# Kernel optimization log

Measured on AMD Instinct MI355X. Metric: run time of the kernel, lower is better.

## Reference

```python
import jax, jax.numpy as jnp
import numpy as np

P, B, D, H, O = 512, 8, 256, 75, 128  # passage_len, batch, input_size, attn hidden, GRU hidden


def setup_inputs() -> dict:
    key = jax.random.key(0)
    ks = jax.random.split(key, 10)

    def w(k, shape, fan_in):
        return jax.random.normal(k, shape, jnp.float32) * (1.0 / np.sqrt(fan_in))

    return {
        "v": jax.random.normal(ks[0], (P, B, D), jnp.float32),
        "Wvp1": w(ks[1], (H, D), D),          # nn.Linear(input_size, hidden, bias=False)
        "Wvp2": w(ks[2], (H, D), D),
        "vw": w(ks[3], (H,), H),               # nn.Linear(hidden, 1, bias=False)
        "Wg": w(ks[4], (2 * D, 2 * D), 2 * D),  # Gate linear, no bias
        "w_ih_f": w(ks[5], (3 * O, 2 * D), 2 * D),
        "w_hh_f": w(ks[6], (3 * O, O), O),
        "b_ih_f": jnp.zeros((3 * O,), jnp.float32),
        "b_hh_f": jnp.zeros((3 * O,), jnp.float32),
        "w_ih_b": w(ks[7], (3 * O, 2 * D), 2 * D),
        "w_hh_b": w(ks[8], (3 * O, O), O),
        "b_ih_b": jnp.zeros((3 * O,), jnp.float32),
        "b_hh_b": jnp.zeros((3 * O,), jnp.float32),
    }


def _gru(x, w_ih, w_hh, b_ih, b_hh):
    # x: (T, B, in) -> hidden states (T, B, O); PyTorch GRU gate order (r, z, n)
    hdim = w_hh.shape[1]
    xp = x @ w_ih.T + b_ih  # precompute input projections: (T, B, 3O)

    def step(h, xp_t):
        gh = h @ w_hh.T + b_hh
        i_r, i_z, i_n = jnp.split(xp_t, 3, axis=-1)
        h_r, h_z, h_n = jnp.split(gh, 3, axis=-1)
        r = jax.nn.sigmoid(i_r + h_r)
        z = jax.nn.sigmoid(i_z + h_z)
        n = jnp.tanh(i_n + r * h_n)
        h_new = (1.0 - z) * n + z * h
        return h_new, h_new

    h0 = jnp.zeros((x.shape[1], hdim), x.dtype)
    _, hs = jax.lax.scan(step, h0, xp)
    return hs


def reference(v, Wvp1, Wvp2, vw, Wg,
              w_ih_f, w_hh_f, b_ih_f, b_hh_f,
              w_ih_b, w_hh_b, b_ih_b, b_hh_b):
    # dropout is inference no-op (and in the torch code its result is discarded anyway)
    Wv1 = v @ Wvp1.T  # (P, B, H) -- broadcast over key axis (dim 1 after expand)
    Wv2 = v @ Wvp2.T  # (P, B, H) -- broadcast over query axis
    # s[i, j, b, h] = tanh(Wv2[i] + Wv1[j]); softmax over i (keys)
    s = jnp.tanh(Wv2[:, None] + Wv1[None, :])          # (P, P, B, H)
    scores = jnp.einsum('ijbh,h->ijb', s, vw)          # (P, P, B)
    a = jax.nn.softmax(scores, axis=0)
    c = jnp.einsum('ijb,ibd->jbd', a, v)               # attended context (P, B, D)
    g = jnp.concatenate([v, c], axis=2)                # (P, B, 2D)
    g = jax.nn.sigmoid(g @ Wg.T) * g                   # Gate
    hf = _gru(g, w_ih_f, w_hh_f, b_ih_f, b_hh_f)
    hb = _gru(g[::-1], w_ih_b, w_hh_b, b_ih_b, b_hh_b)[::-1]
    return jnp.concatenate([hf, hb], axis=2)           # (P, B, 2O)
```

## Files before the change

kernel.cpp:

```cpp
#include <hip/hip_runtime.h>

#define TP 512
#define TB 8
#define TD 256
#define TH 75
#define THP 80
#define TO 128

#define LOG2E2 2.8853900817779268f

typedef _Float16 half_t;
typedef _Float16 half2v __attribute__((ext_vector_type(2)));
typedef _Float16 half4v __attribute__((ext_vector_type(4)));
typedef _Float16 half8v __attribute__((ext_vector_type(8)));
typedef float    float4v __attribute__((ext_vector_type(4)));

__device__ __forceinline__ float fast_rcp(float x) { return __builtin_amdgcn_rcpf(x); }
__device__ __forceinline__ float ex2(float x) {
#if __has_builtin(__builtin_amdgcn_exp2f)
    return __builtin_amdgcn_exp2f(x);
#else
    float r; asm("v_exp_f32 %0, %1" : "=v"(r) : "v"(x)); return r;
#endif
}
__device__ __forceinline__ float fast_tanh(float x) {
    return 1.0f - 2.0f * fast_rcp(1.0f + __expf(2.0f * x));
}
__device__ __forceinline__ float fast_sigmoid(float x) {
    return fast_rcp(1.0f + __expf(-x));
}
__device__ __forceinline__ float fdot2h(half2v a, half2v b, float c) {
#if __has_builtin(__builtin_amdgcn_fdot2)
    return __builtin_amdgcn_fdot2(a, b, c, false);
#else
    return c + (float)a[0] * (float)b[0] + (float)a[1] * (float)b[1];
#endif
}
#define EXT2(v, j) __builtin_shufflevector((v), (v), 2*(j), 2*(j)+1)
__device__ __forceinline__ void dot3_h8(half8v wr, half8v wz, half8v wn, half8v h,
                                        float& ar, float& az, float& an) {
    half2v h0 = EXT2(h, 0), h1 = EXT2(h, 1), h2 = EXT2(h, 2), h3 = EXT2(h, 3);
    ar = fdot2h(EXT2(wr, 0), h0, ar);
    az = fdot2h(EXT2(wz, 0), h0, az);
    an = fdot2h(EXT2(wn, 0), h0, an);
    ar = fdot2h(EXT2(wr, 1), h1, ar);
    az = fdot2h(EXT2(wz, 1), h1, az);
    an = fdot2h(EXT2(wn, 1), h1, an);
    ar = fdot2h(EXT2(wr, 2), h2, ar);
    az = fdot2h(EXT2(wz, 2), h2, az);
    an = fdot2h(EXT2(wn, 2), h2, an);
    ar = fdot2h(EXT2(wr, 3), h3, ar);
    az = fdot2h(EXT2(wz, 3), h3, az);
    an = fdot2h(EXT2(wn, 3), h3, an);
}
__device__ __forceinline__ float pair_sum_dpp(float v) {
    int i1 = __builtin_amdgcn_update_dpp(0, __builtin_bit_cast(int, v), 0xB1, 0xF, 0xF, true);
    return v + __builtin_bit_cast(float, i1);
}

__global__ __launch_bounds__(256) void prep_kernel(
    const float* __restrict__ v,
    const float* __restrict__ Wvp1, const float* __restrict__ Wvp2,
    const float* __restrict__ Wg,   const float* __restrict__ wihf,
    const float* __restrict__ wihb, const float* __restrict__ bihf,
    const float* __restrict__ bihb, const float* __restrict__ whhf,
    const float* __restrict__ whhb,
    float* __restrict__ bihC,
    half_t* __restrict__ v16, half_t* __restrict__ g16,
    half_t* __restrict__ Wg16B, half_t* __restrict__ Wih16B,
    half_t* __restrict__ whh16, half_t* __restrict__ WT16B,
    half_t* __restrict__ vT16)
{
    __shared__ half_t lt[64 * 66];

    if (blockIdx.x >= 7203) {
        int vb = blockIdx.x - 7203;
        int t = threadIdx.x;
        int b  = vb >> 5;
        int pt = (vb >> 2) & 7;
        int dt = vb & 3;
        {
            int pl = t >> 2, dseg = (t & 3) * 16;
            const float4* src = (const float4*)(v + (((pt * 64 + pl) * 8 + b) << 8) + dt * 64 + dseg);
            float4 f0 = src[0], f1 = src[1], f2 = src[2], f3 = src[3];
            half_t hv[16] = {
                (half_t)f0.x,(half_t)f0.y,(half_t)f0.z,(half_t)f0.w,
                (half_t)f1.x,(half_t)f1.y,(half_t)f1.z,(half_t)f1.w,
                (half_t)f2.x,(half_t)f2.y,(half_t)f2.z,(half_t)f2.w,
                (half_t)f3.x,(half_t)f3.y,(half_t)f3.z,(half_t)f3.w };
#pragma unroll
            for (int u = 0; u < 16; ++u) lt[(dseg + u) * 66 + pl] = hv[u];
        }
        __syncthreads();
        {
            int dl = t >> 2, pseg = (t & 3) * 16;
            half8v h0 = *(const half8v*)(lt + dl * 66 + pseg);
            half8v h1 = *(const half8v*)(lt + dl * 66 + pseg + 8);
            half8v* dst = (half8v*)(vT16 + ((b * 256 + dt * 64 + dl) << 9) + pt * 64 + pseg);
            dst[0] = h0; dst[1] = h1;
        }
        return;
    }

    int idx = blockIdx.x * 256 + threadIdx.x;
    if (idx < 1048576) {
        half_t val = (half_t)v[idx];
        v16[idx] = val;
        int row = idx >> 8, d = idx & 255;
        g16[row * 512 + d] = val;
        return;
    }
    idx -= 1048576;
    if (idx < 768) { bihC[idx] = (idx < 384) ? bihf[idx] : bihb[idx - 384]; return; }
    idx -= 768;
    if (idx < 262144) {
        int j = idx & 7, lane = (idx >> 3) & 63, kt = (idx >> 9) & 15, nt = idx >> 13;
        int o = nt * 16 + (lane & 15);
        int k = kt * 32 + ((lane >> 4) << 3) + j;
        Wg16B[idx] = (half_t)Wg[o * 512 + k];
        return;
    }
    idx -= 262144;
    if (idx < 393216) {
        int j = idx & 7, lane = (idx >> 3) & 63, kt = (idx >> 9) & 15, nt = idx >> 13;
        int o = nt * 16 + (lane & 15);
        int k = kt * 32 + ((lane >> 4) << 3) + j;
        Wih16B[idx] = (half_t)((o < 384) ? wihf[o * 512 + k] : wihb[(o - 384) * 512 + k]);
        return;
    }
    idx -= 393216;
    if (idx < 98304) {
        int d = idx / 49152, i = idx - d * 49152;
        whh16[idx] = (half_t)(d ? whhb[i] : whhf[i]);
        return;
    }
    idx -= 98304;
    if (idx < 40960) {
        int j = idx & 7, lane = (idx >> 3) & 63, kt = (idx >> 9) & 7, nt = idx >> 12;
        int o = nt * 16 + (lane & 15);
        int k = kt * 32 + ((lane >> 4) << 3) + j;
        float vv = 0.0f;
        if (o < 75)       vv = Wvp1[o * 256 + k];
        else if (o < 150) vv = Wvp2[(o - 75) * 256 + k];
        WT16B[idx] = (half_t)vv;
    }
}

__global__ __launch_bounds__(128) void wv12_kernel(
    const half_t* __restrict__ v16, const half_t* __restrict__ WT16B,
    float* __restrict__ Wv1, float* __restrict__ Wv2T)
{
    int tid = threadIdx.x;
    int lane = tid & 63, w = tid >> 6;
    int l15 = lane & 15, quad = lane >> 4;
    int r0 = blockIdx.x * 16;

    float4v acc[5];
#pragma unroll
    for (int n5 = 0; n5 < 5; ++n5) acc[n5] = (float4v){0.f, 0.f, 0.f, 0.f};

#pragma unroll
    for (int kt = 0; kt < 8; ++kt) {
        half8v a = *(const half8v*)(v16 + (r0 + l15) * 256 + kt * 32 + quad * 8);
#pragma unroll
        for (int n5 = 0; n5 < 5; ++n5) {
            int nt = w * 5 + n5;
            half8v b = *(const half8v*)(WT16B + ((nt * 8 + kt) * 64 + lane) * 8);
            acc[n5] = __builtin_amdgcn_mfma_f32_16x16x32_f16(a, b, acc[n5], 0, 0, 0);
        }
    }
#pragma unroll
    for (int n5 = 0; n5 < 5; ++n5) {
        int col = (w * 5 + n5) * 16 + l15;
#pragma unroll
        for (int r = 0; r < 4; ++r) {
            int row = r0 + quad * 4 + r;
            int p = row >> 3, b = row & 7;
            int ob = (b * TP + p) * THP;
            float val2 = LOG2E2 * acc[n5][r];
            if (col < 75)       Wv1[ob + col] = val2;
            else if (col < 80)  { Wv1[ob + col] = 0.0f;
                                  Wv2T[(b * THP + col - 75) * TP + p] = val2; }
            else if (col < 150) Wv2T[(b * THP + col - 75) * TP + p] = val2;
            else if (col < 155) Wv2T[(b * THP + col - 75) * TP + p] = 0.0f;
        }
    }
}

__global__ __launch_bounds__(256) void score_kernel(
    const float* __restrict__ Wv1, const float* __restrict__ Wv2T,
    const float* __restrict__ vw, half_t* __restrict__ a16)
{
    int tid = threadIdx.x;
    int b  = blockIdx.x >> 7;
    int j0 = (blockIdx.x & 127) * 4;
    __shared__ float wv1j[4 * THP];
    __shared__ float vws[THP];
    __shared__ float sc[4 * TP];

    if (tid < THP) vws[tid] = (tid < TH) ? vw[tid] : 0.0f;
    for (int e = tid; e < 4 * THP; e += 256) {
        int jj = e / THP, k = e - jj * THP;
        wv1j[e] = Wv1[(b * TP + j0 + jj) * THP + k];
    }
    __syncthreads();

    float Csum = 0.0f;
    {
        const float4* c4 = (const float4*)vws;
        for (int kk = 0; kk < 20; ++kk) { float4 c = c4[kk]; Csum += c.x + c.y + c.z + c.w; }
    }

    int i0 = tid, i1 = tid + 256;
    float acc0[4] = {0.f,0.f,0.f,0.f}, acc1[4] = {0.f,0.f,0.f,0.f};
    const float* wvt = Wv2T + b * THP * TP;
#pragma unroll
    for (int kt = 0; kt < 5; ++kt) {
        float r0v[16], r1v[16];
#pragma unroll
        for (int u = 0; u < 16; ++u) {
            const float* colp = wvt + (kt * 16 + u) * TP;
            r0v[u] = colp[i0];
            r1v[u] = colp[i1];
        }
        const float* cp = vws + kt * 16;
#pragma unroll
        for (int jj = 0; jj < 4; ++jj) {
            const float* w1 = wv1j + jj * THP + kt * 16;
            float s0 = 0.f, s1 = 0.f;
#pragma unroll
            for (int u = 0; u < 16; ++u) {
                float cu = cp[u], wu = w1[u];
                s0 += cu * fast_rcp(1.0f + ex2(r0v[u] + wu));
                s1 += cu * fast_rcp(1.0f + ex2(r1v[u] + wu));
            }
            acc0[jj] += s0; acc1[jj] += s1;
        }
    }
#pragma unroll
    for (int jj = 0; jj < 4; ++jj) {
        sc[jj * TP + i0] = Csum - 2.0f * acc0[jj];
        sc[jj * TP + i1] = Csum - 2.0f * acc1[jj];
    }
    __syncthreads();

    {
        int jj = tid >> 6, l = tid & 63;
        float m = -1e30f;
#pragma unroll
        for (int q = 0; q < 8; ++q) m = fmaxf(m, sc[jj * TP + l + q * 64]);
#pragma unroll
        for (int s = 32; s > 0; s >>= 1) m = fmaxf(m, __shfl_xor(m, s));
        float e[8];
        float sum = 0.0f;
#pragma unroll
        for (int q = 0; q < 8; ++q) { e[q] = __expf(sc[jj * TP + l + q * 64] - m); sum += e[q]; }
#pragma unroll
        for (int s = 32; s > 0; s >>= 1) sum += __shfl_xor(sum, s);
        float inv = fast_rcp(sum);
        half_t* arow = a16 + (b * TP + j0 + jj) * TP;
#pragma unroll
        for (int q = 0; q < 8; ++q) arow[l + q * 64] = (half_t)(e[q] * inv);
    }
}

__global__ __launch_bounds__(256) void context_kernel(
    const half_t* __restrict__ a16, const half_t* __restrict__ vT16,
    half_t* __restrict__ g16)
{
    int tid = threadIdx.x;
    int lane = tid & 63, w = tid >> 6;
    int l15 = lane & 15, quad = lane >> 4;
    int b  = blockIdx.x >> 5;
    int mt = blockIdx.x & 31;

    const half_t* arow = a16 + (b * TP + mt * 16 + l15) * TP;
    const half_t* vbase = vT16 + ((b * 256) << 9);

    float4v acc[4];
#pragma unroll
    for (int nti = 0; nti < 4; ++nti) acc[nti] = (float4v){0.f, 0.f, 0.f, 0.f};

#pragma unroll 4
    for (int kt = 0; kt < 16; ++kt) {
        half8v a = *(const half8v*)(arow + kt * 32 + quad * 8);
#pragma unroll
        for (int nti = 0; nti < 4; ++nti) {
            int d = (w * 4 + nti) * 16 + l15;
            half8v bb = *(const half8v*)(vbase + (d << 9) + kt * 32 + quad * 8);
            acc[nti] = __builtin_amdgcn_mfma_f32_16x16x32_f16(a, bb, acc[nti], 0, 0, 0);
        }
    }
#pragma unroll
    for (int nti = 0; nti < 4; ++nti) {
        int d = (w * 4 + nti) * 16 + l15;
#pragma unroll
        for (int r = 0; r < 4; ++r) {
            int j = mt * 16 + quad * 4 + r;
            g16[(j * TB + b) * 512 + 256 + d] = (half_t)acc[nti][r];
        }
    }
}

__global__ __launch_bounds__(256, 1) void gatexp_kernel(
    const half_t* __restrict__ g16, const half_t* __restrict__ Wg16B,
    const half_t* __restrict__ Wih16B, const float* __restrict__ bihC,
    float* __restrict__ xpf, float* __restrict__ xpb)
{
    __shared__ half_t gA[32 * 520];
    int tid = threadIdx.x;
    int r0 = blockIdx.x * 32;
    int lane = tid & 63, w = tid >> 6;
    int l15 = lane & 15, quad = lane >> 4;

    for (int e = tid; e < 2048; e += 256) {
        int row = e >> 6, c8 = e & 63;
        *(half8v*)(gA + row * 520 + c8 * 8) =
            *(const half8v*)(g16 + (r0 + row) * 512 + c8 * 8);
    }
    __syncthreads();

    float4v acc[2][8];
#pragma unroll
    for (int mi = 0; mi < 2; ++mi)
#pragma unroll
        for (int nti = 0; nti < 8; ++nti) acc[mi][nti] = (float4v){0.f, 0.f, 0.f, 0.f};

    for (int kt = 0; kt < 16; ++kt) {
        half8v a0 = *(const half8v*)(gA + l15 * 520 + kt * 32 + quad * 8);
        half8v a1 = *(const half8v*)(gA + (16 + l15) * 520 + kt * 32 + quad * 8);
#pragma unroll
        for (int nti = 0; nti < 8; ++nti) {
            half8v bb = *(const half8v*)(Wg16B + (((w * 8 + nti) * 16 + kt) * 64 + lane) * 8);
            acc[0][nti] = __builtin_amdgcn_mfma_f32_16x16x32_f16(a0, bb, acc[0][nti], 0, 0, 0);
            acc[1][nti] = __builtin_amdgcn_mfma_f32_16x16x32_f16(a1, bb, acc[1][nti], 0, 0, 0);
        }
    }
#pragma unroll
    for (int mi = 0; mi < 2; ++mi)
#pragma unroll
        for (int nti = 0; nti < 8; ++nti) {
            int colg = (w * 8 + nti) * 16 + l15;
#pragma unroll
            for (int r = 0; r < 4; ++r) {
                float gv = (float)gA[(mi * 16 + quad * 4 + r) * 520 + colg];
                acc[mi][nti][r] = fast_sigmoid(acc[mi][nti][r]) * gv;
            }
        }
    __syncthreads();
#pragma unroll
    for (int mi = 0; mi < 2; ++mi)
#pragma unroll
        for (int nti = 0; nti < 8; ++nti) {
            int colg = (w * 8 + nti) * 16 + l15;
#pragma unroll
            for (int r = 0; r < 4; ++r)
                gA[(mi * 16 + quad * 4 + r) * 520 + colg] = (half_t)acc[mi][nti][r];
        }
    __syncthreads();

    float4v c2[2][12];
#pragma unroll
    for (int mi = 0; mi < 2; ++mi)
#pragma unroll
        for (int nt2 = 0; nt2 < 12; ++nt2) {
            float bv = bihC[(w * 12 + nt2) * 16 + l15];
            c2[mi][nt2] = (float4v){bv, bv, bv, bv};
        }

    for (int kt = 0; kt < 16; ++kt) {
        half8v a0 = *(const half8v*)(gA + l15 * 520 + kt * 32 + quad * 8);
        half8v a1 = *(const half8v*)(gA + (16 + l15) * 520 + kt * 32 + quad * 8);
#pragma unroll
        for (int nt2 = 0; nt2 < 12; ++nt2) {
            half8v bb = *(const half8v*)(Wih16B + (((w * 12 + nt2) * 16 + kt) * 64 + lane) * 8);
            c2[0][nt2] = __builtin_amdgcn_mfma_f32_16x16x32_f16(a0, bb, c2[0][nt2], 0, 0, 0);
            c2[1][nt2] = __builtin_amdgcn_mfma_f32_16x16x32_f16(a1, bb, c2[1][nt2], 0, 0, 0);
        }
    }
#pragma unroll
    for (int mi = 0; mi < 2; ++mi)
#pragma unroll
        for (int nt2 = 0; nt2 < 12; ++nt2) {
            int col = (w * 12 + nt2) * 16 + l15;
            float* dst = (col < 384) ? (xpf + col) : (xpb + col - 384);
#pragma unroll
            for (int r = 0; r < 4; ++r)
                dst[(r0 + mi * 16 + quad * 4 + r) * 384] = c2[mi][nt2][r];
        }
}

__global__ __launch_bounds__(256, 1) void gru_kernel(
    const float* __restrict__ xpf, const float* __restrict__ xpb,
    const half_t* __restrict__ whh16,
    const float* __restrict__ bhhf, const float* __restrict__ bhhb,
    float* __restrict__ out)
{
    int tid = threadIdx.x;
    int dir = blockIdx.x >> 3;
    int b   = blockIdx.x & 7;
    const float* xp  = dir ? xpb  : xpf;
    const float* bhh = dir ? bhhb : bhhf;
    const half_t* wbase = whh16 + dir * 3 * TO * TO;

    __shared__ __align__(16) half_t hb[2][TO];

    int o = tid >> 1, hf = tid & 1;

    half8v wr[8], wz[8], wn[8];
    {
        const half_t* pr = wbase + (o)          * TO + hf * 64;
        const half_t* pz = wbase + (TO + o)     * TO + hf * 64;
        const half_t* pn = wbase + (2 * TO + o) * TO + hf * 64;
        asm volatile(
            "global_load_dwordx4 %0,  %24, off\n\t"
            "global_load_dwordx4 %1,  %24, off offset:16\n\t"
            "global_load_dwordx4 %2,  %24, off offset:32\n\t"
            "global_load_dwordx4 %3,  %24, off offset:48\n\t"
            "global_load_dwordx4 %4,  %24, off offset:64\n\t"
            "global_load_dwordx4 %5,  %24, off offset:80\n\t"
            "global_load_dwordx4 %6,  %24, off offset:96\n\t"
            "global_load_dwordx4 %7,  %24, off offset:112\n\t"
            "global_load_dwordx4 %8,  %25, off\n\t"
            "global_load_dwordx4 %9,  %25, off offset:16\n\t"
            "global_load_dwordx4 %10, %25, off offset:32\n\t"
            "global_load_dwordx4 %11, %25, off offset:48\n\t"
            "global_load_dwordx4 %12, %25, off offset:64\n\t"
            "global_load_dwordx4 %13, %25, off offset:80\n\t"
            "global_load_dwordx4 %14, %25, off offset:96\n\t"
            "global_load_dwordx4 %15, %25, off offset:112\n\t"
            "global_load_dwordx4 %16, %26, off\n\t"
            "global_load_dwordx4 %17, %26, off offset:16\n\t"
            "global_load_dwordx4 %18, %26, off offset:32\n\t"
            "global_load_dwordx4 %19, %26, off offset:48\n\t"
            "global_load_dwordx4 %20, %26, off offset:64\n\t"
            "global_load_dwordx4 %21, %26, off offset:80\n\t"
            "global_load_dwordx4 %22, %26, off offset:96\n\t"
            "global_load_dwordx4 %23, %26, off offset:112\n\t"
            "s_waitcnt vmcnt(0)"
            : "=&v"(wr[0]), "=&v"(wr[1]), "=&v"(wr[2]), "=&v"(wr[3]),
              "=&v"(wr[4]), "=&v"(wr[5]), "=&v"(wr[6]), "=&v"(wr[7]),
              "=&v"(wz[0]), "=&v"(wz[1]), "=&v"(wz[2]), "=&v"(wz[3]),
              "=&v"(wz[4]), "=&v"(wz[5]), "=&v"(wz[6]), "=&v"(wz[7]),
              "=&v"(wn[0]), "=&v"(wn[1]), "=&v"(wn[2]), "=&v"(wn[3]),
              "=&v"(wn[4]), "=&v"(wn[5]), "=&v"(wn[6]), "=&v"(wn[7])
            : "v"(pr), "v"(pz), "v"(pn));
    }

    float br = 0.f, bz = 0.f, bn = 0.f, h = 0.f;
    if (hf == 0) {
        br = bhh[o]; bz = bhh[TO + o]; bn = bhh[2 * TO + o];
    }
    if (tid < TO) hb[0][tid] = (half_t)0.0f;
    __syncthreads();

    float xrv[8], xzv[8], xnv[8], hist[8];

    for (int S = 0; S < TP; S += 8) {
        if (hf == 0) {
#pragma unroll
            for (int u = 0; u < 8; ++u) {
                int s = S + u;
                int tn = dir ? (TP - 1 - s) : s;
                const float* xpt = xp + (tn * TB + b) * 384;
                xrv[u] = xpt[o]; xzv[u] = xpt[TO + o]; xnv[u] = xpt[2 * TO + o];
            }
        }
#pragma unroll
        for (int u = 0; u < 8; ++u) {
            int s = S + u;
            int cur = s & 1;
            const half8v* h8 = (const half8v*)(&hb[cur][hf * 64]);
            half8v hv0 = h8[0], hv1 = h8[1], hv2 = h8[2], hv3 = h8[3];
            half8v hv4 = h8[4], hv5 = h8[5], hv6 = h8[6], hv7 = h8[7];

            float ar = 0.f, az = 0.f, an = 0.f;
            dot3_h8(wr[0], wz[0], wn[0], hv0, ar, az, an);
            dot3_h8(wr[1], wz[1], wn[1], hv1, ar, az, an);
            dot3_h8(wr[2], wz[2], wn[2], hv2, ar, az, an);
            dot3_h8(wr[3], wz[3], wn[3], hv3, ar, az, an);
            dot3_h8(wr[4], wz[4], wn[4], hv4, ar, az, an);
            dot3_h8(wr[5], wz[5], wn[5], hv5, ar, az, an);
            dot3_h8(wr[6], wz[6], wn[6], hv6, ar, az, an);
            dot3_h8(wr[7], wz[7], wn[7], hv7, ar, az, an);

            ar = pair_sum_dpp(ar);
            az = pair_sum_dpp(az);
            an = pair_sum_dpp(an);
            if (hf == 0) {
                float r = fast_sigmoid(xrv[u] + ar + br);
                float z = fast_sigmoid(xzv[u] + az + bz);
                float n = fast_tanh(xnv[u] + r * (an + bn));
                h = (1.0f - z) * n + z * h;
                hb[cur ^ 1][o] = (half_t)h;
                hist[u] = h;
            }
            asm volatile("s_waitcnt lgkmcnt(0)" ::: "memory");
            __builtin_amdgcn_s_barrier();
        }
        if (hf == 0) {
#pragma unroll
            for (int u = 0; u < 8; ++u) {
                int s = S + u;
                int t = dir ? (TP - 1 - s) : s;
                out[(t * TB + b) * 256 + dir * TO + o] = hist[u];
            }
        }
    }
}

extern "C" void kernel_launch(void* const* d_in, const int* in_sizes, int n_in,
                              void* d_out, int out_size, void* d_ws, size_t ws_size,
                              hipStream_t stream) {
    const float* v    = (const float*)d_in[0];
    const float* Wvp1 = (const float*)d_in[1];
    const float* Wvp2 = (const float*)d_in[2];
    const float* vw   = (const float*)d_in[3];
    const float* Wg   = (const float*)d_in[4];
    const float* wihf = (const float*)d_in[5];
    const float* whhf = (const float*)d_in[6];
    const float* bihf = (const float*)d_in[7];
    const float* bhhf = (const float*)d_in[8];
    const float* wihb = (const float*)d_in[9];
    const float* whhb = (const float*)d_in[10];
    const float* bihb = (const float*)d_in[11];
    const float* bhhb = (const float*)d_in[12];

    float* ws   = (float*)d_ws;
    float* bihC = ws;
    float* Wv1  = bihC + 768;
    float* Wv2T = Wv1 + 327680;
    float* xpf  = Wv2T + 327680;
    float* xpb  = xpf + 1572864;
    half_t* g16    = (half_t*)(xpb + 1572864);
    half_t* Wg16B  = g16 + 2097152;
    half_t* Wih16B = Wg16B + 262144;
    half_t* whh16  = Wih16B + 393216;
    half_t* v16    = whh16 + 98304;
    half_t* WT16B  = v16 + 1048576;
    half_t* vT16   = WT16B + 40960;
    half_t* a16    = vT16 + 1048576;
    float* out  = (float*)d_out;

    prep_kernel<<<7459, 256, 0, stream>>>(v, Wvp1, Wvp2, Wg, wihf, wihb, bihf, bihb,
                                          whhf, whhb, bihC, v16, g16,
                                          Wg16B, Wih16B, whh16, WT16B, vT16);
    wv12_kernel<<<256, 128, 0, stream>>>(v16, WT16B, Wv1, Wv2T);
    score_kernel<<<1024, 256, 0, stream>>>(Wv1, Wv2T, vw, a16);
    context_kernel<<<256, 256, 0, stream>>>(a16, vT16, g16);
    gatexp_kernel<<<128, 256, 0, stream>>>(g16, Wg16B, Wih16B, bihC, xpf, xpb);
    gru_kernel<<<16, 256, 0, stream>>>(xpf, xpb, whh16, bhhf, bhhb, out);
}
```

Measured before the change: 417.0 us.

## Fuse attention and gate stages into one persistent kernel with grid barriers

Merges the wv12, score, context and gate/input-projection kernels into a single persistent 512-block kernel that separates the stages with software grid barriers built on atomics. Barrier counters are reset in the prep kernel. The intent is to remove three kernel launch gaps and their tail idle time. In exchange, the kernel depends on all 512 blocks being co-resident, since otherwise the barrier spin deadlocks. Later stages also leave many blocks idle (only 256 or 128 active), and launch_bounds(256,2) may constrain registers.

```diff
diff --git a/kernel.cpp b/kernel.cpp
--- a/kernel.cpp
+++ b/kernel.cpp
@@ -58,6 +58,20 @@
     return v + __builtin_bit_cast(float, i1);
 }
 
+__device__ __forceinline__ void grid_barrier(unsigned* cnt, unsigned* rel, unsigned nblk) {
+    __syncthreads();
+    if (threadIdx.x == 0) {
+        unsigned old = __hip_atomic_fetch_add(cnt, 1u, __ATOMIC_ACQ_REL, __HIP_MEMORY_SCOPE_AGENT);
+        if (old == nblk - 1u) {
+            __hip_atomic_store(rel, 1u, __ATOMIC_RELEASE, __HIP_MEMORY_SCOPE_AGENT);
+        } else {
+            while (__hip_atomic_load(rel, __ATOMIC_ACQUIRE, __HIP_MEMORY_SCOPE_AGENT) == 0u)
+                __builtin_amdgcn_s_sleep(2);
+        }
+    }
+    __syncthreads();
+}
+
 __global__ __launch_bounds__(256) void prep_kernel(
     const float* __restrict__ v,
     const float* __restrict__ Wvp1, const float* __restrict__ Wvp2,
@@ -69,9 +83,11 @@
     half_t* __restrict__ v16, half_t* __restrict__ g16,
     half_t* __restrict__ Wg16B, half_t* __restrict__ Wih16B,
     half_t* __restrict__ whh16, half_t* __restrict__ WT16B,
-    half_t* __restrict__ vT16)
+    half_t* __restrict__ vT16, unsigned* __restrict__ bar)
 {
     __shared__ half_t lt[64 * 66];
+
+    if (blockIdx.x == 0 && threadIdx.x < 8) bar[threadIdx.x] = 0u;
 
     if (blockIdx.x >= 7203) {
         int vb = blockIdx.x - 7203;
@@ -146,248 +162,240 @@
     }
 }
 
-__global__ __launch_bounds__(128) void wv12_kernel(
+__global__ __launch_bounds__(256, 2) void mid_kernel(
     const half_t* __restrict__ v16, const half_t* __restrict__ WT16B,
-    float* __restrict__ Wv1, float* __restrict__ Wv2T)
+    float* __restrict__ Wv1, float* __restrict__ Wv2T,
+    const float* __restrict__ vw, half_t* __restrict__ a16,
+    const half_t* __restrict__ vT16, half_t* __restrict__ g16,
+    const half_t* __restrict__ Wg16B, const half_t* __restrict__ Wih16B,
+    const float* __restrict__ bihC,
+    float* __restrict__ xpf, float* __restrict__ xpb,
+    unsigned* __restrict__ bar)
 {
+    __shared__ __align__(16) unsigned char smem[33280];
     int tid = threadIdx.x;
     int lane = tid & 63, w = tid >> 6;
     int l15 = lane & 15, quad = lane >> 4;
-    int r0 = blockIdx.x * 16;
-
-    float4v acc[5];
-#pragma unroll
-    for (int n5 = 0; n5 < 5; ++n5) acc[n5] = (float4v){0.f, 0.f, 0.f, 0.f};
-
-#pragma unroll
-    for (int kt = 0; kt < 8; ++kt) {
-        half8v a = *(const half8v*)(v16 + (r0 + l15) * 256 + kt * 32 + quad * 8);
-#pragma unroll
-        for (int n5 = 0; n5 < 5; ++n5) {
-            int nt = w * 5 + n5;
-            half8v b = *(const half8v*)(WT16B + ((nt * 8 + kt) * 64 + lane) * 8);
-            acc[n5] = __builtin_amdgcn_mfma_f32_16x16x32_f16(a, b, acc[n5], 0, 0, 0);
-        }
-    }
-#pragma unroll
-    for (int n5 = 0; n5 < 5; ++n5) {
-        int col = (w * 5 + n5) * 16 + l15;
-#pragma unroll
-        for (int r = 0; r < 4; ++r) {
-            int row = r0 + quad * 4 + r;
-            int p = row >> 3, b = row & 7;
-            int ob = (b * TP + p) * THP;
-            float val2 = LOG2E2 * acc[n5][r];
-            if (col < 75)       Wv1[ob + col] = val2;
-            else if (col < 80)  { Wv1[ob + col] = 0.0f;
-                                  Wv2T[(b * THP + col - 75) * TP + p] = val2; }
-            else if (col < 150) Wv2T[(b * THP + col - 75) * TP + p] = val2;
-            else if (col < 155) Wv2T[(b * THP + col - 75) * TP + p] = 0.0f;
-        }
-    }
-}
-
-__global__ __launch_bounds__(256) void score_kernel(
-    const float* __restrict__ Wv1, const float* __restrict__ Wv2T,
-    const float* __restrict__ vw, half_t* __restrict__ a16)
-{
-    int tid = threadIdx.x;
-    int b  = blockIdx.x >> 7;
-    int j0 = (blockIdx.x & 127) * 4;
-    __shared__ float wv1j[4 * THP];
-    __shared__ float vws[THP];
-    __shared__ float sc[4 * TP];
-
-    if (tid < THP) vws[tid] = (tid < TH) ? vw[tid] : 0.0f;
-    for (int e = tid; e < 4 * THP; e += 256) {
-        int jj = e / THP, k = e - jj * THP;
-        wv1j[e] = Wv1[(b * TP + j0 + jj) * THP + k];
-    }
-    __syncthreads();
-
-    float Csum = 0.0f;
+
     {
-        const float4* c4 = (const float4*)vws;
-        for (int kk = 0; kk < 20; ++kk) { float4 c = c4[kk]; Csum += c.x + c.y + c.z + c.w; }
-    }
-
-    int i0 = tid, i1 = tid + 256;
-    float acc0[4] = {0.f,0.f,0.f,0.f}, acc1[4] = {0.f,0.f,0.f,0.f};
-    const float* wvt = Wv2T + b * THP * TP;
-#pragma unroll
-    for (int kt = 0; kt < 5; ++kt) {
-        float r0v[16], r1v[16];
-#pragma unroll
-        for (int u = 0; u < 16; ++u) {
-            const float* colp = wvt + (kt * 16 + u) * TP;
-            r0v[u] = colp[i0];
-            r1v[u] = colp[i1];
-        }
-        const float* cp = vws + kt * 16;
-#pragma unroll
-        for (int jj = 0; jj < 4; ++jj) {
-            const float* w1 = wv1j + jj * THP + kt * 16;
-            float s0 = 0.f, s1 = 0.f;
-#pragma unroll
-            for (int u = 0; u < 16; ++u) {
-                float cu = cp[u], wu = w1[u];
-                s0 += cu * fast_rcp(1.0f + ex2(r0v[u] + wu));
-                s1 += cu * fast_rcp(1.0f + ex2(r1v[u] + wu));
-            }
-            acc0[jj] += s0; acc1[jj] += s1;
-        }
-    }
-#pragma unroll
-    for (int jj = 0; jj < 4; ++jj) {
-        sc[jj * TP + i0] = Csum - 2.0f * acc0[jj];
-        sc[jj * TP + i1] = Csum - 2.0f * acc1[jj];
-    }
-    __syncthreads();
+        int g = blockIdx.x * 4 + w;
+        for (int t = g; t < 2560; t += 2048) {
+            int rt = t / 10, nt = t - rt * 10;
+            int r0 = rt * 16;
+            float4v acc = (float4v){0.f, 0.f, 0.f, 0.f};
+#pragma unroll
+            for (int kt = 0; kt < 8; ++kt) {
+                half8v a = *(const half8v*)(v16 + (r0 + l15) * 256 + kt * 32 + quad * 8);
+                half8v b = *(const half8v*)(WT16B + ((nt * 8 + kt) * 64 + lane) * 8);
+                acc = __builtin_amdgcn_mfma_f32_16x16x32_f16(a, b, acc, 0, 0, 0);
+            }
+            int col = nt * 16 + l15;
+#pragma unroll
+            for (int r = 0; r < 4; ++r) {
+                int row = r0 + quad * 4 + r;
+                int p = row >> 3, b = row & 7;
+                int ob = (b * TP + p) * THP;
+                float val2 = LOG2E2 * acc[r];
+                if (col < 75)       Wv1[ob + col] = val2;
+                else if (col < 80)  { Wv1[ob + col] = 0.0f;
+                                      Wv2T[(b * THP + col - 75) * TP + p] = val2; }
+                else if (col < 150) Wv2T[(b * THP + col - 75) * TP + p] = val2;
+                else if (col < 155) Wv2T[(b * THP + col - 75) * TP + p] = 0.0f;
+            }
+        }
+    }
+    grid_barrier(bar + 0, bar + 1, 512);
 
     {
-        int jj = tid >> 6, l = tid & 63;
-        float m = -1e30f;
-#pragma unroll
-        for (int q = 0; q < 8; ++q) m = fmaxf(m, sc[jj * TP + l + q * 64]);
-#pragma unroll
-        for (int s = 32; s > 0; s >>= 1) m = fmaxf(m, __shfl_xor(m, s));
-        float e[8];
-        float sum = 0.0f;
-#pragma unroll
-        for (int q = 0; q < 8; ++q) { e[q] = __expf(sc[jj * TP + l + q * 64] - m); sum += e[q]; }
-#pragma unroll
-        for (int s = 32; s > 0; s >>= 1) sum += __shfl_xor(sum, s);
-        float inv = fast_rcp(sum);
-        half_t* arow = a16 + (b * TP + j0 + jj) * TP;
-#pragma unroll
-        for (int q = 0; q < 8; ++q) arow[l + q * 64] = (half_t)(e[q] * inv);
-    }
-}
-
-__global__ __launch_bounds__(256) void context_kernel(
-    const half_t* __restrict__ a16, const half_t* __restrict__ vT16,
-    half_t* __restrict__ g16)
-{
-    int tid = threadIdx.x;
-    int lane = tid & 63, w = tid >> 6;
-    int l15 = lane & 15, quad = lane >> 4;
-    int b  = blockIdx.x >> 5;
-    int mt = blockIdx.x & 31;
-
-    const half_t* arow = a16 + (b * TP + mt * 16 + l15) * TP;
-    const half_t* vbase = vT16 + ((b * 256) << 9);
-
-    float4v acc[4];
-#pragma unroll
-    for (int nti = 0; nti < 4; ++nti) acc[nti] = (float4v){0.f, 0.f, 0.f, 0.f};
+        float* wv1j = (float*)smem;
+        float* vws  = wv1j + 4 * THP;
+        float* sc   = vws + THP;
+        for (int t = blockIdx.x; t < 1024; t += 512) {
+            int b  = t >> 7;
+            int j0 = (t & 127) * 4;
+
+            if (tid < THP) vws[tid] = (tid < TH) ? vw[tid] : 0.0f;
+            for (int e = tid; e < 4 * THP; e += 256) {
+                int jj = e / THP, k = e - jj * THP;
+                wv1j[e] = Wv1[(b * TP + j0 + jj) * THP + k];
+            }
+            __syncthreads();
+
+            float Csum = 0.0f;
+            {
+                const float4* c4 = (const float4*)vws;
+                for (int kk = 0; kk < 20; ++kk) { float4 c = c4[kk]; Csum += c.x + c.y + c.z + c.w; }
+            }
+
+            int i0 = tid, i1 = tid + 256;
+            float acc0[4] = {0.f,0.f,0.f,0.f}, acc1[4] = {0.f,0.f,0.f,0.f};
+            const float* wvt = Wv2T + b * THP * TP;
+#pragma unroll
+            for (int kt = 0; kt < 5; ++kt) {
+                float r0v[16], r1v[16];
+#pragma unroll
+                for (int u = 0; u < 16; ++u) {
+                    const float* colp = wvt + (kt * 16 + u) * TP;
+                    r0v[u] = colp[i0];
+                    r1v[u] = colp[i1];
+                }
+                const float* cp = vws + kt * 16;
+#pragma unroll
+                for (int jj = 0; jj < 4; ++jj) {
+                    const float* w1 = wv1j + jj * THP + kt * 16;
+                    float s0 = 0.f, s1 = 0.f;
+#pragma unroll
+                    for (int u = 0; u < 16; ++u) {
+                        float cu = cp[u], wu = w1[u];
+                        s0 += cu * fast_rcp(1.0f + ex2(r0v[u] + wu));
+                        s1 += cu * fast_rcp(1.0f + ex2(r1v[u] + wu));
+                    }
+                    acc0[jj] += s0; acc1[jj] += s1;
+                }
+            }
+#pragma unroll
+            for (int jj = 0; jj < 4; ++jj) {
+                sc[jj * TP + i0] = Csum - 2.0f * acc0[jj];
+                sc[jj * TP + i1] = Csum - 2.0f * acc1[jj];
+            }
+            __syncthreads();
+
+            {
+                int jj = tid >> 6, l = tid & 63;
+                float m = -1e30f;
+#pragma unroll
+                for (int q = 0; q < 8; ++q) m = fmaxf(m, sc[jj * TP + l + q * 64]);
+#pragma unroll
+                for (int s = 32; s > 0; s >>= 1) m = fmaxf(m, __shfl_xor(m, s));
+                float e[8];
+                float sum = 0.0f;
+#pragma unroll
+                for (int q = 0; q < 8; ++q) { e[q] = __expf(sc[jj * TP + l + q * 64] - m); sum += e[q]; }
+#pragma unroll
+                for (int s = 32; s > 0; s >>= 1) sum += __shfl_xor(sum, s);
+                float inv = fast_rcp(sum);
+                half_t* arow = a16 + (b * TP + j0 + jj) * TP;
+#pragma unroll
+                for (int q = 0; q < 8; ++q) arow[l + q * 64] = (half_t)(e[q] * inv);
+            }
+            __syncthreads();
+        }
+    }
+    grid_barrier(bar + 2, bar + 3, 512);
+
+    if (blockIdx.x < 256) {
+        int b  = blockIdx.x >> 5;
+        int mt = blockIdx.x & 31;
+
+        const half_t* arow = a16 + (b * TP + mt * 16 + l15) * TP;
+        const half_t* vbase = vT16 + ((b * 256) << 9);
+
+        float4v acc[4];
+#pragma unroll
+        for (int nti = 0; nti < 4; ++nti) acc[nti] = (float4v){0.f, 0.f, 0.f, 0.f};
 
 #pragma unroll 4
-    for (int kt = 0; kt < 16; ++kt) {
-        half8v a = *(const half8v*)(arow + kt * 32 + quad * 8);
+        for (int kt = 0; kt < 16; ++kt) {
+            half8v a = *(const half8v*)(arow + kt * 32 + quad * 8);
+#pragma unroll
+            for (int nti = 0; nti < 4; ++nti) {
+                int d = (w * 4 + nti) * 16 + l15;
+                half8v bb = *(const half8v*)(vbase + (d << 9) + kt * 32 + quad * 8);
+                acc[nti] = __builtin_amdgcn_mfma_f32_16x16x32_f16(a, bb, acc[nti], 0, 0, 0);
+            }
+        }
 #pragma unroll
         for (int nti = 0; nti < 4; ++nti) {
             int d = (w * 4 + nti) * 16 + l15;
-            half8v bb = *(const half8v*)(vbase + (d << 9) + kt * 32 + quad * 8);
-            acc[nti] = __builtin_amdgcn_mfma_f32_16x16x32_f16(a, bb, acc[nti], 0, 0, 0);
-        }
-    }
-#pragma unroll
-    for (int nti = 0; nti < 4; ++nti) {
-        int d = (w * 4 + nti) * 16 + l15;
-#pragma unroll
-        for (int r = 0; r < 4; ++r) {
-            int j = mt * 16 + quad * 4 + r;
-            g16[(j * TB + b) * 512 + 256 + d] = (half_t)acc[nti][r];
-        }
-    }
-}
-
-__global__ __launch_bounds__(256, 1) void gatexp_kernel(
-    const half_t* __restrict__ g16, const half_t* __restrict__ Wg16B,
-    const half_t* __restrict__ Wih16B, const float* __restrict__ bihC,
-    float* __restrict__ xpf, float* __restrict__ xpb)
-{
-    __shared__ half_t gA[32 * 520];
-    int tid = threadIdx.x;
-    int r0 = blockIdx.x * 32;
-    int lane = tid & 63, w = tid >> 6;
-    int l15 = lane & 15, quad = lane >> 4;
-
-    for (int e = tid; e < 2048; e += 256) {
-        int row = e >> 6, c8 = e & 63;
-        *(half8v*)(gA + row * 520 + c8 * 8) =
-            *(const half8v*)(g16 + (r0 + row) * 512 + c8 * 8);
-    }
-    __syncthreads();
-
-    float4v acc[2][8];
-#pragma unroll
-    for (int mi = 0; mi < 2; ++mi)
-#pragma unroll
-        for (int nti = 0; nti < 8; ++nti) acc[mi][nti] = (float4v){0.f, 0.f, 0.f, 0.f};
-
-    for (int kt = 0; kt < 16; ++kt) {
-        half8v a0 = *(const half8v*)(gA + l15 * 520 + kt * 32 + quad * 8);
-        half8v a1 = *(const half8v*)(gA + (16 + l15) * 520 + kt * 32 + quad * 8);
-#pragma unroll
-        for (int nti = 0; nti < 8; ++nti) {
-            half8v bb = *(const half8v*)(Wg16B + (((w * 8 + nti) * 16 + kt) * 64 + lane) * 8);
-            acc[0][nti] = __builtin_amdgcn_mfma_f32_16x16x32_f16(a0, bb, acc[0][nti], 0, 0, 0);
-            acc[1][nti] = __builtin_amdgcn_mfma_f32_16x16x32_f16(a1, bb, acc[1][nti], 0, 0, 0);
-        }
-    }
-#pragma unroll
-    for (int mi = 0; mi < 2; ++mi)
-#pragma unroll
-        for (int nti = 0; nti < 8; ++nti) {
-            int colg = (w * 8 + nti) * 16 + l15;
 #pragma unroll
             for (int r = 0; r < 4; ++r) {
-                float gv = (float)gA[(mi * 16 + quad * 4 + r) * 520 + colg];
-                acc[mi][nti][r] = fast_sigmoid(acc[mi][nti][r]) * gv;
-            }
-        }
-    __syncthreads();
-#pragma unroll
-    for (int mi = 0; mi < 2; ++mi)
-#pragma unroll
-        for (int nti = 0; nti < 8; ++nti) {
-            int colg = (w * 8 + nti) * 16 + l15;
-#pragma unroll
-            for (int r = 0; r < 4; ++r)
-                gA[(mi * 16 + quad * 4 + r) * 520 + colg] = (half_t)acc[mi][nti][r];
-        }
-    __syncthreads();
-
-    float4v c2[2][12];
-#pragma unroll
-    for (int mi = 0; mi < 2; ++mi)
-#pragma unroll
-        for (int nt2 = 0; nt2 < 12; ++nt2) {
-            float bv = bihC[(w * 12 + nt2) * 16 + l15];
-            c2[mi][nt2] = (float4v){bv, bv, bv, bv};
-        }
-
-    for (int kt = 0; kt < 16; ++kt) {
-        half8v a0 = *(const half8v*)(gA + l15 * 520 + kt * 32 + quad * 8);
-        half8v a1 = *(const half8v*)(gA + (16 + l15) * 520 + kt * 32 + quad * 8);
-#pragma unroll
-        for (int nt2 = 0; nt2 < 12; ++nt2) {
-            half8v bb = *(const half8v*)(Wih16B + (((w * 12 + nt2) * 16 + kt) * 64 + lane) * 8);
-            c2[0][nt2] = __builtin_amdgcn_mfma_f32_16x16x32_f16(a0, bb, c2[0][nt2], 0, 0, 0);
-            c2[1][nt2] = __builtin_amdgcn_mfma_f32_16x16x32_f16(a1, bb, c2[1][nt2], 0, 0, 0);
-        }
-    }
-#pragma unroll
-    for (int mi = 0; mi < 2; ++mi)
-#pragma unroll
-        for (int nt2 = 0; nt2 < 12; ++nt2) {
-            int col = (w * 12 + nt2) * 16 + l15;
-            float* dst = (col < 384) ? (xpf + col) : (xpb + col - 384);
-#pragma unroll
-            for (int r = 0; r < 4; ++r)
-                dst[(r0 + mi * 16 + quad * 4 + r) * 384] = c2[mi][nt2][r];
-        }
+                int j = mt * 16 + quad * 4 + r;
+                g16[(j * TB + b) * 512 + 256 + d] = (half_t)acc[nti][r];
+            }
+        }
+    }
+    grid_barrier(bar + 4, bar + 5, 512);
+
+    if (blockIdx.x < 128) {
+        half_t* gA = (half_t*)smem;
+        int r0 = blockIdx.x * 32;
+
+        for (int e = tid; e < 2048; e += 256) {
+            int row = e >> 6, c8 = e & 63;
+            *(half8v*)(gA + row * 520 + c8 * 8) =
+                *(const half8v*)(g16 + (r0 + row) * 512 + c8 * 8);
+        }
+        __syncthreads();
+
+        float4v acc[2][8];
+#pragma unroll
+        for (int mi = 0; mi < 2; ++mi)
+#pragma unroll
+            for (int nti = 0; nti < 8; ++nti) acc[mi][nti] = (float4v){0.f, 0.f, 0.f, 0.f};
+
+        for (int kt = 0; kt < 16; ++kt) {
+            half8v a0 = *(const half8v*)(gA + l15 * 520 + kt * 32 + quad * 8);
+            half8v a1 = *(const half8v*)(gA + (16 + l15) * 520 + kt * 32 + quad * 8);
+#pragma unroll
+            for (int nti = 0; nti < 8; ++nti) {
+                half8v bb = *(const half8v*)(Wg16B + (((w * 8 + nti) * 16 + kt) * 64 + lane) * 8);
+                acc[0][nti] = __builtin_amdgcn_mfma_f32_16x16x32_f16(a0, bb, acc[0][nti], 0, 0, 0);
+                acc[1][nti] = __builtin_amdgcn_mfma_f32_16x16x32_f16(a1, bb, acc[1][nti], 0, 0, 0);
+            }
+        }
+#pragma unroll
+        for (int mi = 0; mi < 2; ++mi)
+#pragma unroll
+            for (int nti = 0; nti < 8; ++nti) {
+                int colg = (w * 8 + nti) * 16 + l15;
+#pragma unroll
+                for (int r = 0; r < 4; ++r) {
+                    float gv = (float)gA[(mi * 16 + quad * 4 + r) * 520 + colg];
+                    acc[mi][nti][r] = fast_sigmoid(acc[mi][nti][r]) * gv;
+                }
+            }
+        __syncthreads();
+#pragma unroll
+        for (int mi = 0; mi < 2; ++mi)
+#pragma unroll
+            for (int nti = 0; nti < 8; ++nti) {
+                int colg = (w * 8 + nti) * 16 + l15;
+#pragma unroll
+                for (int r = 0; r < 4; ++r)
+                    gA[(mi * 16 + quad * 4 + r) * 520 + colg] = (half_t)acc[mi][nti][r];
+            }
+        __syncthreads();
+
+        float4v c2[2][12];
+#pragma unroll
+        for (int mi = 0; mi < 2; ++mi)
+#pragma unroll
+            for (int nt2 = 0; nt2 < 12; ++nt2) {
+                float bv = bihC[(w * 12 + nt2) * 16 + l15];
+                c2[mi][nt2] = (float4v){bv, bv, bv, bv};
+            }
+
+        for (int kt = 0; kt < 16; ++kt) {
+            half8v a0 = *(const half8v*)(gA + l15 * 520 + kt * 32 + quad * 8);
+            half8v a1 = *(const half8v*)(gA + (16 + l15) * 520 + kt * 32 + quad * 8);
+#pragma unroll
+            for (int nt2 = 0; nt2 < 12; ++nt2) {
+                half8v bb = *(const half8v*)(Wih16B + (((w * 12 + nt2) * 16 + kt) * 64 + lane) * 8);
+                c2[0][nt2] = __builtin_amdgcn_mfma_f32_16x16x32_f16(a0, bb, c2[0][nt2], 0, 0, 0);
+                c2[1][nt2] = __builtin_amdgcn_mfma_f32_16x16x32_f16(a1, bb, c2[1][nt2], 0, 0, 0);
+            }
+        }
+#pragma unroll
+        for (int mi = 0; mi < 2; ++mi)
+#pragma unroll
+            for (int nt2 = 0; nt2 < 12; ++nt2) {
+                int col = (w * 12 + nt2) * 16 + l15;
+                float* dst = (col < 384) ? (xpf + col) : (xpb + col - 384);
+#pragma unroll
+                for (int r = 0; r < 4; ++r)
+                    dst[(r0 + mi * 16 + quad * 4 + r) * 384] = c2[mi][nt2][r];
+            }
+    }
 }
 
 __global__ __launch_bounds__(256, 1) void gru_kernel(
@@ -540,14 +548,14 @@
     half_t* WT16B  = v16 + 1048576;
     half_t* vT16   = WT16B + 40960;
     half_t* a16    = vT16 + 1048576;
+    unsigned* bar  = (unsigned*)(a16 + 2097152);
     float* out  = (float*)d_out;
 
     prep_kernel<<<7459, 256, 0, stream>>>(v, Wvp1, Wvp2, Wg, wihf, wihb, bihf, bihb,
                                           whhf, whhb, bihC, v16, g16,
-                                          Wg16B, Wih16B, whh16, WT16B, vT16);
-    wv12_kernel<<<256, 128, 0, stream>>>(v16, WT16B, Wv1, Wv2T);
-    score_kernel<<<1024, 256, 0, stream>>>(Wv1, Wv2T, vw, a16);
-    context_kernel<<<256, 256, 0, stream>>>(a16, vT16, g16);
-    gatexp_kernel<<<128, 256, 0, stream>>>(g16, Wg16B, Wih16B, bihC, xpf, xpb);
+                                          Wg16B, Wih16B, whh16, WT16B, vT16, bar);
+    mid_kernel<<<512, 256, 0, stream>>>(v16, WT16B, Wv1, Wv2T, vw, a16,
+                                        vT16, g16, Wg16B, Wih16B, bihC,
+                                        xpf, xpb, bar);
     gru_kernel<<<16, 256, 0, stream>>>(xpf, xpb, whh16, bhhf, bhhb, out);
 }
```

Result: slower. 628.8 us (+50.8%).
